# Kernel tuning notes

Hardware: AMD Instinct MI355X
Metric: run time of the kernel (lower is better)

Reference implementation:

```python
import jax, jax.numpy as jnp
import numpy as np

DIM = 1024
HEADS = 16
HEAD_DIM = DIM // HEADS
HIDDEN = 4096
EPS = 1e-5


def _layer_norm(x, w, b):
    mu = jnp.mean(x, axis=-1, keepdims=True)
    var = jnp.var(x, axis=-1, keepdims=True)
    return (x - mu) * jax.lax.rsqrt(var + EPS) * w + b


def setup_inputs() -> dict:
    key = jax.random.key(0)
    ks = jax.random.split(key, 16)
    s = lambda fan_in: 1.0 / np.sqrt(fan_in)
    return {
        "x": jax.random.normal(ks[0], (8, 1024, DIM), dtype=jnp.float32),
        "ln1_w": jnp.ones((DIM,), jnp.float32),
        "ln1_b": jnp.zeros((DIM,), jnp.float32),
        "qkv_w": jax.random.uniform(ks[1], (3 * DIM, DIM), jnp.float32, -s(DIM), s(DIM)),
        "qkv_b": jax.random.uniform(ks[2], (3 * DIM,), jnp.float32, -s(DIM), s(DIM)),
        "out_w": jax.random.uniform(ks[3], (DIM, DIM), jnp.float32, -s(DIM), s(DIM)),
        "out_b": jax.random.uniform(ks[4], (DIM,), jnp.float32, -s(DIM), s(DIM)),
        "ln2_w": jnp.ones((DIM,), jnp.float32),
        "ln2_b": jnp.zeros((DIM,), jnp.float32),
        "fc1_w": jax.random.uniform(ks[5], (HIDDEN, DIM), jnp.float32, -s(DIM), s(DIM)),
        "fc1_b": jax.random.uniform(ks[6], (HIDDEN,), jnp.float32, -s(DIM), s(DIM)),
        "fc2_w": jax.random.uniform(ks[7], (DIM, HIDDEN), jnp.float32, -s(HIDDEN), s(HIDDEN)),
        "fc2_b": jax.random.uniform(ks[8], (DIM,), jnp.float32, -s(HIDDEN), s(HIDDEN)),
    }


def reference(x, ln1_w, ln1_b, qkv_w, qkv_b, out_w, out_b,
              ln2_w, ln2_b, fc1_w, fc1_b, fc2_w, fc2_b):
    B, S, D = x.shape
    # --- attention sub-block (pre-LN) ---
    h = _layer_norm(x, ln1_w, ln1_b)
    qkv = h @ qkv_w.T + qkv_b                              # [B,S,3D]
    qkv = qkv.reshape(B, S, 3, HEADS, HEAD_DIM)
    q, k, v = qkv[:, :, 0], qkv[:, :, 1], qkv[:, :, 2]     # [B,S,H,hd]
    scores = jnp.einsum('bqhd,bkhd->bhqk', q, k) / np.sqrt(HEAD_DIM)
    attn = jax.nn.softmax(scores, axis=-1)
    o = jnp.einsum('bhqk,bkhd->bqhd', attn, v).reshape(B, S, D)
    x = x + (o @ out_w.T + out_b)
    # --- MLP sub-block (pre-LN) ---
    h = _layer_norm(x, ln2_w, ln2_b)
    h = jax.nn.gelu(h @ fc1_w.T + fc1_b, approximate=False)
    x = x + (h @ fc2_w.T + fc2_b)
    return x
```

## Files before the change

### kernel.cpp

```cpp
#include <hip/hip_runtime.h>
#include <hip/hip_bf16.h>

typedef unsigned short u16;
typedef __bf16 bf16x8 __attribute__((ext_vector_type(8)));
typedef float f32x4 __attribute__((ext_vector_type(4)));
typedef u16 u16x8 __attribute__((ext_vector_type(8)));
typedef unsigned u32x2 __attribute__((ext_vector_type(2)));

#define LOG2E 1.4426950408889634f
#define QSCALE 0.18033688011112042f

template <int V> struct ic { static constexpr int v = V; };

__device__ __forceinline__ float fast_exp2(float x) {
#if __has_builtin(__builtin_amdgcn_exp2f)
  return __builtin_amdgcn_exp2f(x);
#else
  return exp2f(x);
#endif
}

__device__ __forceinline__ u16 f2bf(float f) {
  union { float f; unsigned u; } c; c.f = f;
  unsigned r = c.u + 0x7fffu + ((c.u >> 16) & 1u);
  return (u16)(r >> 16);
}

__device__ __forceinline__ unsigned pk_bf16(float a, float b) {
#if __has_builtin(__builtin_amdgcn_cvt_pk_bf16_f32)
  typedef __bf16 bf16x2_t __attribute__((ext_vector_type(2)));
  union { bf16x2_t v; unsigned u; } c;
  c.v = __builtin_amdgcn_cvt_pk_bf16_f32(a, b);
  return c.u;
#else
  return (unsigned)f2bf(a) | ((unsigned)f2bf(b) << 16);
#endif
}

__device__ __forceinline__ unsigned pk_bf16_fast(float a, float b) {
#if __has_builtin(__builtin_amdgcn_cvt_pk_bf16_f32)
  return pk_bf16(a, b);
#else
  union { float f; unsigned u; } ca, cb;
  ca.f = a; cb.f = b;
  return __builtin_amdgcn_perm(cb.u, ca.u, 0x07060302u);
#endif
}

__device__ __forceinline__ float gelu_f(float v) {
  float z = 0.7978845608f * v + 0.0356774081f * (v * v * v);
  float e = fast_exp2(z * 2.885390082f);
  float t = 1.0f - 2.0f * __builtin_amdgcn_rcpf(e + 1.0f);
  return 0.5f * v * (1.0f + t);
}

__device__ __forceinline__ void async16(const void* g, void* l) {
  __builtin_amdgcn_global_load_lds(
      (const __attribute__((address_space(1))) void*)g,
      (__attribute__((address_space(3))) void*)l, 16, 0, 0);
}

#define CFENCE asm volatile("" ::: "memory")
#define VMCNT(N) do { asm volatile("s_waitcnt vmcnt(" #N ")" ::: "memory"); \
                      __builtin_amdgcn_sched_barrier(0); } while (0)

__global__ __launch_bounds__(256) void cvt4_kernel(
    const float* __restrict__ s0, const float* __restrict__ s1,
    const float* __restrict__ s2, const float* __restrict__ s3,
    u16* __restrict__ d0, u16* __restrict__ d1,
    u16* __restrict__ d2, u16* __restrict__ d3) {
  int i = blockIdx.x * 256 + threadIdx.x;
  const float* s; u16* d; int off;
  if (i < 786432)       { s = s0; d = d0; off = i; }
  else if (i < 1048576) { s = s1; d = d1; off = i - 786432; }
  else if (i < 2097152) { s = s2; d = d2; off = i - 1048576; }
  else                  { s = s3; d = d3; off = i - 2097152; }
  float4 v = ((const float4*)s)[off];
  ushort4 o;
  o.x = f2bf(v.x); o.y = f2bf(v.y); o.z = f2bf(v.z); o.w = f2bf(v.w);
  ((ushort4*)d)[off] = o;
}

__global__ __launch_bounds__(256) void ln_kernel(const float* __restrict__ x,
                                                 const float* __restrict__ w,
                                                 const float* __restrict__ b,
                                                 u16* __restrict__ out) {
  int row = blockIdx.x;
  int tid = threadIdx.x;
  int lane = tid & 63, wave = tid >> 6;
  float4 v = ((const float4*)(x + (size_t)row * 1024))[tid];
  float s = v.x + v.y + v.z + v.w;
  float s2 = v.x*v.x + v.y*v.y + v.z*v.z + v.w*v.w;
  #pragma unroll
  for (int off = 1; off < 64; off <<= 1) {
    s += __shfl_xor(s, off, 64);
    s2 += __shfl_xor(s2, off, 64);
  }
  __shared__ float red[8];
  if (lane == 0) { red[wave] = s; red[4 + wave] = s2; }
  __syncthreads();
  float st = red[0] + red[1] + red[2] + red[3];
  float s2t = red[4] + red[5] + red[6] + red[7];
  float mu = st * (1.0f / 1024.0f);
  float var = s2t * (1.0f / 1024.0f) - mu * mu;
  float rs = rsqrtf(var + 1e-5f);
  float4 wv = ((const float4*)w)[tid];
  float4 bv = ((const float4*)b)[tid];
  ushort4 o;
  o.x = f2bf((v.x - mu) * rs * wv.x + bv.x);
  o.y = f2bf((v.y - mu) * rs * wv.y + bv.y);
  o.z = f2bf((v.z - mu) * rs * wv.z + bv.z);
  o.w = f2bf((v.w - mu) * rs * wv.w + bv.w);
  ((ushort4*)(out + (size_t)row * 1024))[tid] = o;
}

template <int EPI, int BM, int BN, int NBLOG2>
__global__ __launch_bounds__(512, 2) void gemm8(const u16* __restrict__ A,
                                                const u16* __restrict__ B,
                                                const float* __restrict__ bias,
                                                void* __restrict__ Cout,
                                                const float* __restrict__ resid,
                                                int M, int N, int K) {
  (void)M;
  constexpr int FMH = BM / 64;
  constexpr int FNH = BN / 128;
  constexpr int LA = BM / 128;
  constexpr int LB = BN / 128;
  __shared__ u16 As[2][BM * 64];
  __shared__ u16 Bs[2][BN * 64];
  const int tid = threadIdx.x;
  const int lane = tid & 63, wave = tid >> 6;
  const int wr = wave & 1, wc = wave >> 1;
  const int l15 = lane & 15, l4 = lane >> 4;
  const int nt = K >> 6;

  int m0, n0;
  if constexpr (NBLOG2 < 0) {
    m0 = blockIdx.y * BM; n0 = blockIdx.x * BN;
  } else {
    const int id = blockIdx.x;
    const int xcd = id & 7, slot = id >> 3;
    m0 = ((slot >> NBLOG2) * 8 + xcd) * BM;
    n0 = (slot & ((1 << NBLOG2) - 1)) * BN;
  }

  const int srow = lane >> 3;
  const int sg = (lane & 7) ^ srow;
  const u16* Ab = A + (size_t)(m0 + srow) * K + sg * 8;
  const u16* Bb = B + (size_t)(n0 + srow) * K + sg * 8;

  auto stageA = [&](int tile, int half, int wb) {
    if (tile >= nt) return;
    #pragma unroll
    for (int t = 0; t < LA; t++) {
      const int r0 = half * (BM / 2) + wave * (BM / 16) + t * 8;
      async16(Ab + (size_t)r0 * K + tile * 64, &As[wb][r0 * 64]);
    }
  };
  auto stageB = [&](int tile, int half, int wb) {
    if (tile >= nt) return;
    #pragma unroll
    for (int t = 0; t < LB; t++) {
      const int r0 = half * (BN / 2) + wave * (BN / 16) + t * 8;
      async16(Bb + (size_t)r0 * K + tile * 64, &Bs[wb][r0 * 64]);
    }
  };

  bf16x8 afr[FMH][2];
  bf16x8 bfr[2][FNH][2];

  auto loadA = [&](int rb, auto half_) {
    constexpr int half = decltype(half_)::v;
    #pragma unroll
    for (int f = 0; f < FMH; f++)
      #pragma unroll
      for (int ks = 0; ks < 2; ks++) {
        const int row = half * (BM / 2) + wr * (BM / 4) + f * 16 + l15;
        const int sl = (ks * 4 + l4) ^ (l15 & 7);
        afr[f][ks] = *(const bf16x8*)&As[rb][row * 64 + sl * 8];
      }
  };
  auto loadB = [&](int rb, auto half_) {
    constexpr int half = decltype(half_)::v;
    #pragma unroll
    for (int f = 0; f < FNH; f++)
      #pragma unroll
      for (int ks = 0; ks < 2; ks++) {
        const int col = half * (BN / 2) + wc * (BN / 8) + f * 16 + l15;
        const int sl = (ks * 4 + l4) ^ (l15 & 7);
        bfr[half][f][ks] = *(const bf16x8*)&Bs[rb][col * 64 + sl * 8];
      }
  };

  f32x4 acc[2][FMH][2][FNH];
  #pragma unroll
  for (int a = 0; a < 2; a++)
    #pragma unroll
    for (int f = 0; f < FMH; f++)
      #pragma unroll
      for (int c = 0; c < 2; c++)
        #pragma unroll
        for (int g = 0; g < FNH; g++) {
          f32x4 z = {0.f, 0.f, 0.f, 0.f};
          acc[a][f][c][g] = z;
        }

  auto phase = [&](auto qa_, auto qb_, auto pre, auto stage) {
    constexpr int qa = decltype(qa_)::v;
    constexpr int qb = decltype(qb_)::v;
    pre();
    stage();
    CFENCE;
    __builtin_amdgcn_s_barrier();
    asm volatile("s_waitcnt lgkmcnt(0)" ::: "memory");
    __builtin_amdgcn_sched_barrier(0);
    __builtin_amdgcn_s_setprio(1);
    #pragma unroll
    for (int f = 0; f < FMH; f++)
      #pragma unroll
      for (int g = 0; g < FNH; g++)
        #pragma unroll
        for (int ks = 0; ks < 2; ks++)
          acc[qa][f][qb][g] = __builtin_amdgcn_mfma_f32_16x16x32_bf16(
              afr[f][ks], bfr[qb][g][ks], acc[qa][f][qb][g], 0, 0, 0);
    __builtin_amdgcn_s_setprio(0);
    __builtin_amdgcn_sched_barrier(0);
  };

  auto endphase = [&](int mode) {
    if (mode == 1) {
      if constexpr (LA + LB == 4) VMCNT(4); else VMCNT(3);
    } else if (mode == 2) {
      VMCNT(0);
    }
    CFENCE;
    __builtin_amdgcn_s_barrier();
  };

  stageA(0, 0, 0); stageB(0, 0, 0); stageA(0, 1, 0); stageB(0, 1, 0);
  stageA(1, 0, 1); stageB(1, 0, 1);
  if constexpr (LA + LB == 4) VMCNT(4); else VMCNT(3);
  CFENCE;
  __builtin_amdgcn_s_barrier();

  const int niter = nt >> 1;
  for (int it = 0; it < niter; ++it) {
    const int T = 2 * it;
    const int f4 = (T + 2 < nt) ? 1 : 2;
    const int f8 = (T + 3 < nt) ? 1 : 2;
    phase(ic<0>{}, ic<0>{}, [&]{ loadA(0, ic<0>{}); loadB(0, ic<0>{}); },
          [&]{ stageA(T + 1, 1, 1); }); endphase(0);
    phase(ic<0>{}, ic<1>{}, [&]{ loadB(0, ic<1>{}); },
          [&]{ stageB(T + 1, 1, 1); }); endphase(0);
    phase(ic<1>{}, ic<0>{}, [&]{ loadA(0, ic<1>{}); },
          [&]{ stageA(T + 2, 0, 0); }); endphase(0);
    phase(ic<1>{}, ic<1>{}, [&]{},
          [&]{ stageB(T + 2, 0, 0); }); endphase(f4);
    phase(ic<0>{}, ic<0>{}, [&]{ loadA(1, ic<0>{}); loadB(1, ic<0>{}); },
          [&]{ stageA(T + 2, 1, 0); }); endphase(0);
    phase(ic<0>{}, ic<1>{}, [&]{ loadB(1, ic<1>{}); },
          [&]{ stageB(T + 2, 1, 0); }); endphase(0);
    phase(ic<1>{}, ic<0>{}, [&]{ loadA(1, ic<1>{}); },
          [&]{ stageA(T + 3, 0, 1); }); endphase(0);
    phase(ic<1>{}, ic<1>{}, [&]{},
          [&]{ stageB(T + 3, 0, 1); }); endphase(f8);
  }

  float bv[2][FNH];
  #pragma unroll
  for (int qb = 0; qb < 2; qb++)
    #pragma unroll
    for (int fn = 0; fn < FNH; fn++)
      bv[qb][fn] = bias[n0 + qb * (BN / 2) + wc * (BN / 8) + fn * 16 + l15];

  #pragma unroll
  for (int qa = 0; qa < 2; qa++)
    #pragma unroll
    for (int fm = 0; fm < FMH; fm++) {
      const size_t row0 =
          (size_t)(m0 + qa * (BM / 2) + wr * (BM / 4) + fm * 16 + l4 * 4);
      #pragma unroll
      for (int r = 0; r < 4; r += 2)
        #pragma unroll
        for (int qb = 0; qb < 2; qb++)
          #pragma unroll
          for (int fn = 0; fn < FNH; fn++) {
            const int col = n0 + qb * (BN / 2) + wc * (BN / 8) + fn * 16 + l15;
            float v0 = acc[qa][fm][qb][fn][r] + bv[qb][fn];
            float v1 = acc[qa][fm][qb][fn][r + 1] + bv[qb][fn];
            if (EPI == 1) { v0 = gelu_f(v0); v1 = gelu_f(v1); }
            if (EPI == 3) {
              float sc = (col < 1024) ? QSCALE : 1.0f;
              v0 *= sc; v1 *= sc;
            }
            const size_t off0 = (row0 + r) * (size_t)N + col;
            const size_t off1 = (row0 + r + 1) * (size_t)N + col;
            if (EPI == 2) {
              ((float*)Cout)[off0] = v0 + resid[off0];
              ((float*)Cout)[off1] = v1 + resid[off1];
            } else {
              unsigned pk = pk_bf16(v0, v1);
              ((u16*)Cout)[off0] = (u16)pk;
              ((u16*)Cout)[off1] = (u16)(pk >> 16);
            }
          }
    }
}

__global__ __launch_bounds__(256) void vtrans_kernel(const u16* __restrict__ qkv,
                                                     u16* __restrict__ vtg) {
  const int sc = blockIdx.x, h = blockIdx.y, b = blockIdx.z;
  const int tid = threadIdx.x;
  __shared__ u16 t[64][72];
  const u16* vp = qkv + ((size_t)b * 1024) * 3072 + h * 64 + 2048;
  #pragma unroll
  for (int it = 0; it < 2; it++) {
    int idx = it * 256 + tid;
    int row = idx >> 3, g = idx & 7;
    *(u16x8*)&t[row][g * 8] =
        *(const u16x8*)(vp + (size_t)(sc * 64 + row) * 3072 + g * 8);
  }
  __syncthreads();
  u16* dst = vtg + ((size_t)(b * 16 + h) * 64) * 1024;
  #pragma unroll
  for (int it = 0; it < 2; it++) {
    int idx = it * 256 + tid;
    int d = idx >> 3, g = idx & 7;
    u16x8 o;
    #pragma unroll
    for (int j = 0; j < 8; j++) o[j] = t[g * 8 + j][d];
    *(u16x8*)(dst + (size_t)d * 1024 + sc * 64 + g * 8) = o;
  }
}

__global__ __launch_bounds__(256) void attn_kernel(const u16* __restrict__ qkv,
                                                   const u16* __restrict__ vtg,
                                                   u16* __restrict__ obuf) {
  const int S = 1024, QKV = 3072;
  const int id = blockIdx.x;
  const int qt = id >> 7, hb = id & 127;
  const int h = hb & 15, b = hb >> 4;
  const int tid = threadIdx.x, lane = tid & 63, wave = tid >> 6;
  const int l15 = lane & 15, l4 = lane >> 4;
  const size_t tok0 = (size_t)b * S;
  const u16* qp = qkv + tok0 * QKV + h * 64;
  const u16* kp = qp + 1024;
  const u16* vtp = vtg + (size_t)(b * 16 + h) * 64 * 1024;
  const int q0 = qt * 128;

  __shared__ u16 Ks[128 * 64];
  __shared__ u16 Vt[64 * 128];
  __shared__ u16 Ps[4][16 * 136];

  const u16* qrow = qp + (size_t)(q0 + wave * 16 + l15) * QKV;
  bf16x8 qf[2][2];
  #pragma unroll
  for (int qs = 0; qs < 2; qs++)
    #pragma unroll
    for (int kb = 0; kb < 2; kb++)
      qf[qs][kb] = *(const bf16x8*)(qrow + (size_t)qs * 64 * QKV + kb * 32 + l4 * 8);

  bf16x8 ones;
  #pragma unroll
  for (int j = 0; j < 8; j++) ones[j] = (__bf16)1.0f;

  const int krow = lane >> 3;
  const int klg = (lane & 7) ^ (lane >> 3);
  const int vrow_i = lane >> 4;
  const int vpg = lane & 15;

  f32x4 oacc[2][4], lacc[2];
  #pragma unroll
  for (int qs = 0; qs < 2; qs++) {
    #pragma unroll
    for (int ct = 0; ct < 4; ct++) {
      f32x4 z = {0.f, 0.f, 0.f, 0.f};
      oacc[qs][ct] = z;
    }
    f32x4 z = {0.f, 0.f, 0.f, 0.f};
    lacc[qs] = z;
  }

  for (int j0 = 0; j0 < S; j0 += 128) {
    __syncthreads();
    #pragma unroll
    for (int t = 0; t < 4; t++) {
      int e = wave * 4 + t;
      async16(kp + (size_t)(j0 + e * 8 + krow) * QKV + klg * 8, Ks + e * 512);
    }
    #pragma unroll
    for (int t = 0; t < 4; t++) {
      int e = wave * 4 + t;
      int row = e * 4 + vrow_i;
      int lg = vpg ^ (row & 15);
      async16(vtp + (size_t)row * 1024 + j0 + lg * 8, Vt + e * 512);
    }
    __syncthreads();

    #pragma unroll
    for (int qs = 0; qs < 2; qs++) {
      f32x4 s[8];
      #pragma unroll
      for (int tg = 0; tg < 8; tg++) {
        f32x4 z = {0.f, 0.f, 0.f, 0.f};
        s[tg] = z;
        #pragma unroll
        for (int kb = 0; kb < 2; kb++) {
          int pg = (kb * 4 + l4) ^ (l15 & 7);
          bf16x8 kf = *(const bf16x8*)&Ks[(tg * 16 + l15) * 64 + pg * 8];
          s[tg] = __builtin_amdgcn_mfma_f32_16x16x32_bf16(kf, qf[qs][kb], s[tg], 0, 0, 0);
        }
      }

      #pragma unroll
      for (int tg = 0; tg < 8; tg++)
        #pragma unroll
        for (int r = 0; r < 4; r++)
          s[tg][r] = fast_exp2(s[tg][r]);

      #pragma unroll
      for (int tg = 0; tg < 8; tg++) {
        u32x2 pr;
        pr[0] = pk_bf16_fast(s[tg][0], s[tg][1]);
        pr[1] = pk_bf16_fast(s[tg][2], s[tg][3]);
        *(u32x2*)&Ps[wave][l15 * 136 + tg * 16 + l4 * 4] = pr;
      }
      bf16x8 pf[4];
      #pragma unroll
      for (int kb = 0; kb < 4; kb++)
        pf[kb] = *(const bf16x8*)&Ps[wave][l15 * 136 + kb * 32 + l4 * 8];

      #pragma unroll
      for (int kb = 0; kb < 4; kb++) {
        #pragma unroll
        for (int ct = 0; ct < 4; ct++) {
          int pg = (kb * 4 + l4) ^ l15;
          bf16x8 vf = *(const bf16x8*)&Vt[(ct * 16 + l15) * 128 + pg * 8];
          oacc[qs][ct] = __builtin_amdgcn_mfma_f32_16x16x32_bf16(
              pf[kb], vf, oacc[qs][ct], 0, 0, 0);
        }
        lacc[qs] = __builtin_amdgcn_mfma_f32_16x16x32_bf16(
            pf[kb], ones, lacc[qs], 0, 0, 0);
      }
    }
  }

  #pragma unroll
  for (int qs = 0; qs < 2; qs++) {
    float inv[4];
    #pragma unroll
    for (int r = 0; r < 4; r++) inv[r] = 1.0f / lacc[qs][r];
    #pragma unroll
    for (int ct = 0; ct < 4; ct++)
      #pragma unroll
      for (int r = 0; r < 4; r++) {
        float v = oacc[qs][ct][r] * inv[r];
        size_t row = tok0 + q0 + qs * 64 + wave * 16 + l4 * 4 + r;
        obuf[row * 1024 + h * 64 + ct * 16 + l15] = f2bf(v);
      }
  }
}

extern "C" void kernel_launch(void* const* d_in, const int* in_sizes, int n_in,
                              void* d_out, int out_size, void* d_ws, size_t ws_size,
                              hipStream_t stream) {
  (void)in_sizes; (void)n_in; (void)out_size; (void)ws_size;
  const float* x     = (const float*)d_in[0];
  const float* ln1_w = (const float*)d_in[1];
  const float* ln1_b = (const float*)d_in[2];
  const float* qkv_w = (const float*)d_in[3];
  const float* qkv_b = (const float*)d_in[4];
  const float* out_w = (const float*)d_in[5];
  const float* out_b = (const float*)d_in[6];
  const float* ln2_w = (const float*)d_in[7];
  const float* ln2_b = (const float*)d_in[8];
  const float* fc1_w = (const float*)d_in[9];
  const float* fc1_b = (const float*)d_in[10];
  const float* fc2_w = (const float*)d_in[11];
  const float* fc2_b = (const float*)d_in[12];
  float* out = (float*)d_out;

  char* ws = (char*)d_ws;
  u16* wqkv = (u16*)(ws);
  u16* wout = (u16*)(ws + 6291456);
  u16* wfc1 = (u16*)(ws + 8388608);
  u16* wfc2 = (u16*)(ws + 16777216);
  u16* hbuf = (u16*)(ws + 25165824);
  u16* qbuf = (u16*)(ws + 41943040);
  u16* vtg  = (u16*)(ws + 92274688);

  const int M = 8192;

  cvt4_kernel<<<dim3(12288), 256, 0, stream>>>(qkv_w, out_w, fc1_w, fc2_w,
                                               wqkv, wout, wfc1, wfc2);

  ln_kernel<<<dim3(M), 256, 0, stream>>>(x, ln1_w, ln1_b, hbuf);
  gemm8<3, 128, 256, -1><<<dim3(3072 / 256, M / 128), 512, 0, stream>>>(
      hbuf, wqkv, qkv_b, qbuf, nullptr, M, 3072, 1024);
  vtrans_kernel<<<dim3(16, 16, 8), 256, 0, stream>>>(qbuf, vtg);
  attn_kernel<<<dim3(1024), 256, 0, stream>>>(qbuf, vtg, hbuf);
  gemm8<2, 128, 256, -1><<<dim3(1024 / 256, M / 128), 512, 0, stream>>>(
      hbuf, wout, out_b, out, x, M, 1024, 1024);
  ln_kernel<<<dim3(M), 256, 0, stream>>>(out, ln2_w, ln2_b, hbuf);
  gemm8<1, 256, 256, 4><<<dim3((M / 256) * (4096 / 256)), 512, 0, stream>>>(
      hbuf, wfc1, fc1_b, qbuf, nullptr, M, 4096, 1024);
  gemm8<2, 128, 256, 2><<<dim3((M / 128) * (1024 / 256)), 512, 0, stream>>>(
      qbuf, wfc2, fc2_b, out, out, M, 1024, 4096);
}
```

Measured before the change: 474.3 us.

## Merge GEMM main-loop phases from eight to four per iteration

The GEMM main loop is restructured so each phase computes both N-halves for one M-half, halving the number of phases and the barriers between them. Each phase now issues both the A and B global-to-LDS stage operations together and loads both B fragment halves up front. This cuts barrier and wait overhead and gives the scheduler longer MFMA runs. The cost is more live B fragment registers and burstier memory issue per phase.

```diff
diff --git a/kernel.cpp b/kernel.cpp
--- a/kernel.cpp
+++ b/kernel.cpp
@@ -205,9 +205,8 @@
           acc[a][f][c][g] = z;
         }
 
-  auto phase = [&](auto qa_, auto qb_, auto pre, auto stage) {
+  auto phase = [&](auto qa_, auto pre, auto stage, int endv) {
     constexpr int qa = decltype(qa_)::v;
-    constexpr int qb = decltype(qb_)::v;
     pre();
     stage();
     CFENCE;
@@ -218,19 +217,18 @@
     #pragma unroll
     for (int f = 0; f < FMH; f++)
       #pragma unroll
-      for (int g = 0; g < FNH; g++)
+      for (int qb = 0; qb < 2; qb++)
         #pragma unroll
-        for (int ks = 0; ks < 2; ks++)
-          acc[qa][f][qb][g] = __builtin_amdgcn_mfma_f32_16x16x32_bf16(
-              afr[f][ks], bfr[qb][g][ks], acc[qa][f][qb][g], 0, 0, 0);
+        for (int g = 0; g < FNH; g++)
+          #pragma unroll
+          for (int ks = 0; ks < 2; ks++)
+            acc[qa][f][qb][g] = __builtin_amdgcn_mfma_f32_16x16x32_bf16(
+                afr[f][ks], bfr[qb][g][ks], acc[qa][f][qb][g], 0, 0, 0);
     __builtin_amdgcn_s_setprio(0);
     __builtin_amdgcn_sched_barrier(0);
-  };
-
-  auto endphase = [&](int mode) {
-    if (mode == 1) {
+    if (endv == 1) {
       if constexpr (LA + LB == 4) VMCNT(4); else VMCNT(3);
-    } else if (mode == 2) {
+    } else if (endv == 2) {
       VMCNT(0);
     }
     CFENCE;
@@ -246,24 +244,20 @@
   const int niter = nt >> 1;
   for (int it = 0; it < niter; ++it) {
     const int T = 2 * it;
-    const int f4 = (T + 2 < nt) ? 1 : 2;
-    const int f8 = (T + 3 < nt) ? 1 : 2;
-    phase(ic<0>{}, ic<0>{}, [&]{ loadA(0, ic<0>{}); loadB(0, ic<0>{}); },
-          [&]{ stageA(T + 1, 1, 1); }); endphase(0);
-    phase(ic<0>{}, ic<1>{}, [&]{ loadB(0, ic<1>{}); },
-          [&]{ stageB(T + 1, 1, 1); }); endphase(0);
-    phase(ic<1>{}, ic<0>{}, [&]{ loadA(0, ic<1>{}); },
-          [&]{ stageA(T + 2, 0, 0); }); endphase(0);
-    phase(ic<1>{}, ic<1>{}, [&]{},
-          [&]{ stageB(T + 2, 0, 0); }); endphase(f4);
-    phase(ic<0>{}, ic<0>{}, [&]{ loadA(1, ic<0>{}); loadB(1, ic<0>{}); },
-          [&]{ stageA(T + 2, 1, 0); }); endphase(0);
-    phase(ic<0>{}, ic<1>{}, [&]{ loadB(1, ic<1>{}); },
-          [&]{ stageB(T + 2, 1, 0); }); endphase(0);
-    phase(ic<1>{}, ic<0>{}, [&]{ loadA(1, ic<1>{}); },
-          [&]{ stageA(T + 3, 0, 1); }); endphase(0);
-    phase(ic<1>{}, ic<1>{}, [&]{},
-          [&]{ stageB(T + 3, 0, 1); }); endphase(f8);
+    const int f2 = (T + 2 < nt) ? 1 : 2;
+    const int f4 = (T + 3 < nt) ? 1 : 2;
+    phase(ic<0>{},
+          [&]{ loadA(0, ic<0>{}); loadB(0, ic<0>{}); loadB(0, ic<1>{}); },
+          [&]{ stageA(T + 1, 1, 1); stageB(T + 1, 1, 1); }, 0);
+    phase(ic<1>{},
+          [&]{ loadA(0, ic<1>{}); },
+          [&]{ stageA(T + 2, 0, 0); stageB(T + 2, 0, 0); }, f2);
+    phase(ic<0>{},
+          [&]{ loadA(1, ic<0>{}); loadB(1, ic<0>{}); loadB(1, ic<1>{}); },
+          [&]{ stageA(T + 2, 1, 0); stageB(T + 2, 1, 0); }, 0);
+    phase(ic<1>{},
+          [&]{ loadA(1, ic<1>{}); },
+          [&]{ stageA(T + 3, 0, 1); stageB(T + 3, 0, 1); }, f4);
   }
 
   float bv[2][FNH];
```

Measured after the change: 481.2 us. No clear change (+1.5%).
